# Kernel optimization log

Measured on AMD Instinct MI355X. Metric: run time of the kernel, lower is better.

The kernel has to match this reference:

```python
import jax, jax.numpy as jnp
import numpy as np

N = 50000      # nodes
E = 800000     # edges
IN = 128       # in_ch
OUT = 32       # out_ch
H = 4          # heads
ED = 16        # edge_dim
SLOPE = 0.2    # LeakyReLU negative slope (GATv2 default and outer activation)


def setup_inputs() -> dict:
    key = jax.random.key(0)
    ks = jax.random.split(key, 10)
    s_in = 1.0 / np.sqrt(IN)
    s_ed = 1.0 / np.sqrt(ED)
    s_out = 1.0 / np.sqrt(OUT)
    return {
        "x": jax.random.normal(ks[0], (N, IN), jnp.float32),
        "edge_index": jax.random.randint(ks[1], (2, E), 0, N, dtype=jnp.int32),
        "edges_attr": jax.random.normal(ks[2], (E, ED), jnp.float32),
        "W_l": jax.random.normal(ks[3], (IN, H * OUT), jnp.float32) * s_in,
        "b_l": jnp.zeros((H * OUT,), jnp.float32),
        "W_r": jax.random.normal(ks[4], (IN, H * OUT), jnp.float32) * s_in,
        "b_r": jnp.zeros((H * OUT,), jnp.float32),
        "W_e": jax.random.normal(ks[5], (ED, H * OUT), jnp.float32) * s_ed,
        "att": jax.random.normal(ks[6], (H, OUT), jnp.float32) * s_out,
        "bias": jnp.zeros((OUT,), jnp.float32),
    }


def reference(x, edge_index, edges_attr, W_l, b_l, W_r, b_r, W_e, att, bias):
    src, tgt = edge_index[0], edge_index[1]

    # add_self_loops with fill_value='mean': self-loop attr = scatter-mean of
    # incoming edge attrs per target node (0 for isolated nodes, as in PyG).
    deg = jax.ops.segment_sum(jnp.ones((E,), x.dtype), tgt, num_segments=N)
    attr_sum = jax.ops.segment_sum(edges_attr, tgt, num_segments=N)
    loop_attr = attr_sum / jnp.maximum(deg, 1.0)[:, None]
    node_ids = jnp.arange(N, dtype=src.dtype)
    src_f = jnp.concatenate([src, node_ids])   # [E+N]
    tgt_f = jnp.concatenate([tgt, node_ids])   # [E+N]
    attr_f = jnp.concatenate([edges_attr, loop_attr], axis=0)  # [E+N, ED]

    x_l = (x @ W_l + b_l).reshape(N, H, OUT)   # source transform
    x_r = (x @ W_r + b_r).reshape(N, H, OUT)   # target transform
    e = (attr_f @ W_e).reshape(-1, H, OUT)     # edge transform

    # GATv2 score: att . leaky_relu(x_l[j] + x_r[i] + e_ij)
    m = x_l[src_f] + x_r[tgt_f] + e                          # [E+N, H, OUT]
    scores = jnp.einsum('ehc,hc->eh', jax.nn.leaky_relu(m, SLOPE), att)

    # scatter-softmax over edges grouped by target node (every segment has a
    # self-loop, so segment_max is well-defined)
    smax = jax.ops.segment_max(scores, tgt_f, num_segments=N)
    ex = jnp.exp(scores - smax[tgt_f])
    denom = jax.ops.segment_sum(ex, tgt_f, num_segments=N)
    alpha = ex / denom[tgt_f]                                # [E+N, H]

    # weighted aggregation of source messages x_l[j]
    msg = alpha[:, :, None] * x_l[src_f]                     # [E+N, H, OUT]
    out = jax.ops.segment_sum(msg, tgt_f, num_segments=N)   # [N, H, OUT]

    out = out.mean(axis=1) + bias                            # concat=False -> head mean
    return jax.nn.leaky_relu(out, SLOPE)                     # outer LeakyReLU(0.2)
```

## Files before the change

### kernel.cpp

```cpp
#include <hip/hip_runtime.h>
#include <math.h>

#define NN 50000
#define NE 800000
#define SLOPE 0.2f
#define NB 49
#define GEMMB 782
#define EDGEB 3125

typedef __attribute__((ext_vector_type(8))) short bf16x8;
typedef __attribute__((ext_vector_type(4))) float f32x4;

static __device__ __forceinline__ void split_bf16(float v, unsigned short& h,
                                                  unsigned short& l) {
  unsigned u = __float_as_uint(v);
  h = (unsigned short)(u >> 16);
  float hf = __uint_as_float(((unsigned)h) << 16);
  float r = v - hf;
  l = (unsigned short)(__float_as_uint(r) >> 16);
}


__device__ __forceinline__ void gemm_body(int bx, const float* __restrict__ x,
                                          const float* __restrict__ W,
                                          const float* __restrict__ bptr,
                                          float* __restrict__ optr,
                                          unsigned short* xh_s, unsigned short* xl_s,
                                          unsigned short* wh_s, unsigned short* wl_s) {
  int tid = threadIdx.x;
  int w = tid >> 6;
  int l = tid & 63;
  int n0 = bx * 64;

  f32x4 acc[8];
#pragma unroll
  for (int i = 0; i < 8; ++i) acc[i] = (f32x4){0.f, 0.f, 0.f, 0.f};

  for (int kb = 0; kb < 128; kb += 32) {
    {
      int row = tid >> 2;
      int kc = (tid & 3) * 8;
      int gn = n0 + row;
      float4 v0 = make_float4(0.f, 0.f, 0.f, 0.f);
      float4 v1 = make_float4(0.f, 0.f, 0.f, 0.f);
      if (gn < NN) {
        v0 = *(const float4*)(x + (size_t)gn * 128 + kb + kc);
        v1 = *(const float4*)(x + (size_t)gn * 128 + kb + kc + 4);
      }
      unsigned short h[8], lo[8];
      split_bf16(v0.x, h[0], lo[0]); split_bf16(v0.y, h[1], lo[1]);
      split_bf16(v0.z, h[2], lo[2]); split_bf16(v0.w, h[3], lo[3]);
      split_bf16(v1.x, h[4], lo[4]); split_bf16(v1.y, h[5], lo[5]);
      split_bf16(v1.z, h[6], lo[6]); split_bf16(v1.w, h[7], lo[7]);
      bf16x8 hv, lv;
#pragma unroll
      for (int i = 0; i < 8; ++i) { hv[i] = (short)h[i]; lv[i] = (short)lo[i]; }
      *(bf16x8*)&xh_s[row * 40 + kc] = hv;
      *(bf16x8*)&xl_s[row * 40 + kc] = lv;
    }
    {
      int col = tid & 127;
      int kk0 = (tid >> 7) * 16;
      unsigned short h[16], lo[16];
#pragma unroll
      for (int j = 0; j < 16; ++j)
        split_bf16(W[(size_t)(kb + kk0 + j) * 128 + col], h[j], lo[j]);
      bf16x8 hv0, hv1, lv0, lv1;
#pragma unroll
      for (int i = 0; i < 8; ++i) {
        hv0[i] = (short)h[i]; hv1[i] = (short)h[8 + i];
        lv0[i] = (short)lo[i]; lv1[i] = (short)lo[8 + i];
      }
      *(bf16x8*)&wh_s[col * 40 + kk0] = hv0;
      *(bf16x8*)&wh_s[col * 40 + kk0 + 8] = hv1;
      *(bf16x8*)&wl_s[col * 40 + kk0] = lv0;
      *(bf16x8*)&wl_s[col * 40 + kk0 + 8] = lv1;
    }
    __syncthreads();

    int r16 = 16 * w + (l & 15);
    int ko = (l >> 4) * 8;
    bf16x8 ah = *(bf16x8*)&xh_s[r16 * 40 + ko];
    bf16x8 al = *(bf16x8*)&xl_s[r16 * 40 + ko];
#pragma unroll
    for (int ct = 0; ct < 8; ++ct) {
      int cbase = (ct * 16 + (l & 15)) * 40 + ko;
      bf16x8 bh = *(bf16x8*)&wh_s[cbase];
      bf16x8 bl = *(bf16x8*)&wl_s[cbase];
      acc[ct] = __builtin_amdgcn_mfma_f32_16x16x32_bf16(ah, bh, acc[ct], 0, 0, 0);
      acc[ct] = __builtin_amdgcn_mfma_f32_16x16x32_bf16(al, bh, acc[ct], 0, 0, 0);
      acc[ct] = __builtin_amdgcn_mfma_f32_16x16x32_bf16(ah, bl, acc[ct], 0, 0, 0);
    }
    __syncthreads();
  }

  int colb = l & 15;
  int rq = (l >> 4) * 4;
#pragma unroll
  for (int ct = 0; ct < 8; ++ct) {
    float bvv = bptr[ct * 16 + colb];
#pragma unroll
    for (int r = 0; r < 4; ++r) {
      int gn = n0 + 16 * w + rq + r;
      if (gn < NN) optr[(size_t)gn * 128 + ct * 16 + colb] = acc[ct][r] + bvv;
    }
  }
}


__launch_bounds__(256)
__global__ void fusedA_kernel(const float* __restrict__ x,
                              const float* __restrict__ W_l, const float* __restrict__ b_l,
                              float* __restrict__ x_l,
                              const int* __restrict__ tgt, int* __restrict__ deg,
                              int* __restrict__ rank) {
  __shared__ unsigned short xh_s[64 * 40], xl_s[64 * 40];
  __shared__ unsigned short wh_s[128 * 40], wl_s[128 * 40];
  if (blockIdx.x < GEMMB) {
    gemm_body(blockIdx.x, x, W_l, b_l, x_l, xh_s, xl_s, wh_s, wl_s);
  } else {
    int e = (blockIdx.x - GEMMB) * 256 + threadIdx.x;
    if (e < NE) rank[e] = atomicAdd(&deg[tgt[e]], 1);
  }
}


__launch_bounds__(256)
__global__ void fusedB_kernel(const float* __restrict__ x,
                              const float* __restrict__ W_r, const float* __restrict__ b_r,
                              float* __restrict__ x_r,
                              const int* __restrict__ src, const int* __restrict__ tgt,
                              const int* __restrict__ rank,
                              const int* __restrict__ rowptr,
                              const float4* __restrict__ eattr4,
                              int* __restrict__ csr_src,
                              float4* __restrict__ eattr_csr4) {
  __shared__ unsigned short xh_s[64 * 40], xl_s[64 * 40];
  __shared__ unsigned short wh_s[128 * 40], wl_s[128 * 40];
  if (blockIdx.x < GEMMB) {
    gemm_body(blockIdx.x, x, W_r, b_r, x_r, xh_s, xl_s, wh_s, wl_s);
  } else {
    int e = (blockIdx.x - GEMMB) * 256 + threadIdx.x;
    if (e < NE) {
      int t = tgt[e];
      int r = rank[e];
      float4 a0 = eattr4[(size_t)e * 4 + 0];
      float4 a1 = eattr4[(size_t)e * 4 + 1];
      float4 a2 = eattr4[(size_t)e * 4 + 2];
      float4 a3 = eattr4[(size_t)e * 4 + 3];
      int pos = rowptr[t] + r;
      csr_src[pos] = src[e];
      eattr_csr4[(size_t)pos * 4 + 0] = a0;
      eattr_csr4[(size_t)pos * 4 + 1] = a1;
      eattr_csr4[(size_t)pos * 4 + 2] = a2;
      eattr_csr4[(size_t)pos * 4 + 3] = a3;
    }
  }
}


__global__ void partial_kernel(const int* __restrict__ deg, int* __restrict__ psum) {
  int b = blockIdx.x;
  int base = b * 1024 + threadIdx.x * 4;
  int s = 0;
  if (base + 3 < NN) {
    int4 v = *(const int4*)(deg + base);
    s = v.x + v.y + v.z + v.w;
  } else {
#pragma unroll
    for (int i = 0; i < 4; ++i)
      if (base + i < NN) s += deg[base + i];
  }
  s += __shfl_xor(s, 1);
  s += __shfl_xor(s, 2);
  s += __shfl_xor(s, 4);
  s += __shfl_xor(s, 8);
  s += __shfl_xor(s, 16);
  s += __shfl_xor(s, 32);
  __shared__ int wsum[4];
  if ((threadIdx.x & 63) == 0) wsum[threadIdx.x >> 6] = s;
  __syncthreads();
  if (threadIdx.x == 0) psum[b] = wsum[0] + wsum[1] + wsum[2] + wsum[3];
}

__global__ void final_kernel(const int* __restrict__ deg, const int* __restrict__ psum,
                             int* __restrict__ rowptr) {
  __shared__ int offs_s;
  __shared__ int wtot[4];
  int b = blockIdx.x;
  int t = threadIdx.x;
  if (t < 64) {
    int lane = t;
    int mine = (lane < NB) ? psum[lane] : 0;
    int v = mine;
#pragma unroll
    for (int off = 1; off < 64; off <<= 1) {
      int u = __shfl_up(v, off);
      if (lane >= off) v += u;
    }
    if (lane == b) offs_s = v - mine;
    if (b == 0 && lane == 63) rowptr[NN] = v;
  }
  __syncthreads();

  int base = b * 1024 + t * 4;
  int d0 = 0, d1 = 0, d2 = 0, d3 = 0;
  if (base + 3 < NN) {
    int4 v = *(const int4*)(deg + base);
    d0 = v.x; d1 = v.y; d2 = v.z; d3 = v.w;
  } else {
    if (base < NN) d0 = deg[base];
    if (base + 1 < NN) d1 = deg[base + 1];
    if (base + 2 < NN) d2 = deg[base + 2];
  }
  int s = d0 + d1 + d2 + d3;
  int lane = t & 63, w = t >> 6;
  int v = s;
#pragma unroll
  for (int off = 1; off < 64; off <<= 1) {
    int u = __shfl_up(v, off);
    if (lane >= off) v += u;
  }
  if (lane == 63) wtot[w] = v;
  __syncthreads();
  int woff = 0;
#pragma unroll
  for (int i = 0; i < 4; ++i)
    if (i < w) woff += wtot[i];
  int run = offs_s + woff + (v - s);
  if (base < NN)     { rowptr[base] = run;     run += d0; }
  if (base + 1 < NN) { rowptr[base + 1] = run; run += d1; }
  if (base + 2 < NN) { rowptr[base + 2] = run; run += d2; }
  if (base + 3 < NN) { rowptr[base + 3] = run; }
}


#define EDGE_PROC(AV, XL)                                              \
  {                                                                    \
    float e0 = AV[0] * wek[0].x;                                       \
    e0 = fmaf(AV[1], wek[1].x, e0);   e0 = fmaf(AV[2], wek[2].x, e0);  \
    e0 = fmaf(AV[3], wek[3].x, e0);   e0 = fmaf(AV[4], wek[4].x, e0);  \
    e0 = fmaf(AV[5], wek[5].x, e0);   e0 = fmaf(AV[6], wek[6].x, e0);  \
    e0 = fmaf(AV[7], wek[7].x, e0);   e0 = fmaf(AV[8], wek[8].x, e0);  \
    e0 = fmaf(AV[9], wek[9].x, e0);   e0 = fmaf(AV[10], wek[10].x, e0);\
    e0 = fmaf(AV[11], wek[11].x, e0); e0 = fmaf(AV[12], wek[12].x, e0);\
    e0 = fmaf(AV[13], wek[13].x, e0); e0 = fmaf(AV[14], wek[14].x, e0);\
    e0 = fmaf(AV[15], wek[15].x, e0);                                  \
    float e1 = AV[0] * wek[0].y;                                       \
    e1 = fmaf(AV[1], wek[1].y, e1);   e1 = fmaf(AV[2], wek[2].y, e1);  \
    e1 = fmaf(AV[3], wek[3].y, e1);   e1 = fmaf(AV[4], wek[4].y, e1);  \
    e1 = fmaf(AV[5], wek[5].y, e1);   e1 = fmaf(AV[6], wek[6].y, e1);  \
    e1 = fmaf(AV[7], wek[7].y, e1);   e1 = fmaf(AV[8], wek[8].y, e1);  \
    e1 = fmaf(AV[9], wek[9].y, e1);   e1 = fmaf(AV[10], wek[10].y, e1);\
    e1 = fmaf(AV[11], wek[11].y, e1); e1 = fmaf(AV[12], wek[12].y, e1);\
    e1 = fmaf(AV[13], wek[13].y, e1); e1 = fmaf(AV[14], wek[14].y, e1);\
    e1 = fmaf(AV[15], wek[15].y, e1);                                  \
    es0 += e0; es1 += e1;                                              \
    float m0 = (XL.x + xr.x) + e0;                                     \
    float m1 = (XL.y + xr.y) + e1;                                     \
    float lm0 = fmaf(SLOPE, fminf(m0, 0.f), fmaxf(m0, 0.f));           \
    float lm1 = fmaf(SLOPE, fminf(m1, 0.f), fmaxf(m1, 0.f));           \
    float part = fmaf(attv.y, lm1, attv.x * lm0);                      \
    part += __shfl_xor(part, 1);                                       \
    part += __shfl_xor(part, 2);                                       \
    part += __shfl_xor(part, 4);                                       \
    part += __shfl_xor(part, 8);                                       \
    float p = __expf(part);                                            \
    lh += p;                                                           \
    acc0 = fmaf(p, XL.x, acc0);                                        \
    acc1 = fmaf(p, XL.y, acc1);                                        \
  }

__launch_bounds__(256)
__global__ void gat_kernel(const float* __restrict__ x_l, const float* __restrict__ x_r,
                           const int* __restrict__ rowptr, const int* __restrict__ csr_src,
                           const float* __restrict__ eattr_csr, const float* __restrict__ W_e,
                           const float* __restrict__ att, const float* __restrict__ bias,
                           float* __restrict__ out) {
  int wid = threadIdx.x >> 6;
  int lane = threadIdx.x & 63;
  int tbase = (blockIdx.x * 4 + wid) * 4;

  float2 wek[16];
#pragma unroll
  for (int k = 0; k < 16; ++k)
    wek[k] = *(const float2*)(W_e + k * 128 + 2 * lane);
  float2 attv = *(const float2*)(att + 2 * lane);
  float bv = bias[(2 * lane) & 31];
  float bv1 = bias[((2 * lane) & 31) + 1];

  for (int tt = 0; tt < 4; ++tt) {
    int t = tbase + tt;
    float2 xr = *(const float2*)(x_r + (size_t)t * 128 + 2 * lane);
    int start = __builtin_amdgcn_readfirstlane(rowptr[t]);
    int end = __builtin_amdgcn_readfirstlane(rowptr[t + 1]);

    float lh = 0.f, acc0 = 0.f, acc1 = 0.f, es0 = 0.f, es1 = 0.f;

    int j = start;
    for (; j + 4 <= end; j += 4) {
      int s0 = __builtin_amdgcn_readfirstlane(csr_src[j]);
      int s1 = __builtin_amdgcn_readfirstlane(csr_src[j + 1]);
      int s2 = __builtin_amdgcn_readfirstlane(csr_src[j + 2]);
      int s3 = __builtin_amdgcn_readfirstlane(csr_src[j + 3]);
      float2 xl0 = *(const float2*)(x_l + (size_t)s0 * 128 + 2 * lane);
      float2 xl1 = *(const float2*)(x_l + (size_t)s1 * 128 + 2 * lane);
      float2 xl2 = *(const float2*)(x_l + (size_t)s2 * 128 + 2 * lane);
      float2 xl3 = *(const float2*)(x_l + (size_t)s3 * 128 + 2 * lane);
      const float* ap0 = eattr_csr + (size_t)j * 16;
      {
        float a0[16];
#pragma unroll
        for (int k = 0; k < 16; ++k) a0[k] = ap0[k];
        EDGE_PROC(a0, xl0)
      }
      {
        float a1[16];
#pragma unroll
        for (int k = 0; k < 16; ++k) a1[k] = ap0[16 + k];
        EDGE_PROC(a1, xl1)
      }
      {
        float a2[16];
#pragma unroll
        for (int k = 0; k < 16; ++k) a2[k] = ap0[32 + k];
        EDGE_PROC(a2, xl2)
      }
      {
        float a3[16];
#pragma unroll
        for (int k = 0; k < 16; ++k) a3[k] = ap0[48 + k];
        EDGE_PROC(a3, xl3)
      }
    }
    if (j + 2 <= end) {
      int s0 = __builtin_amdgcn_readfirstlane(csr_src[j]);
      int s1 = __builtin_amdgcn_readfirstlane(csr_src[j + 1]);
      float2 xl0 = *(const float2*)(x_l + (size_t)s0 * 128 + 2 * lane);
      float2 xl1 = *(const float2*)(x_l + (size_t)s1 * 128 + 2 * lane);
      const float* ap0 = eattr_csr + (size_t)j * 16;
      {
        float a0[16];
#pragma unroll
        for (int k = 0; k < 16; ++k) a0[k] = ap0[k];
        EDGE_PROC(a0, xl0)
      }
      {
        float a1[16];
#pragma unroll
        for (int k = 0; k < 16; ++k) a1[k] = ap0[16 + k];
        EDGE_PROC(a1, xl1)
      }
      j += 2;
    }
    if (j < end) {
      int srcn = __builtin_amdgcn_readfirstlane(csr_src[j]);
      const float* ap = eattr_csr + (size_t)j * 16;
      float aC[16];
#pragma unroll
      for (int k = 0; k < 16; ++k) aC[k] = ap[k];
      float2 xlC = *(const float2*)(x_l + (size_t)srcn * 128 + 2 * lane);
      EDGE_PROC(aC, xlC)
    }

    {
      float rdeg = 1.0f / fmaxf((float)(end - start), 1.0f);
      float e0 = es0 * rdeg, e1 = es1 * rdeg;
      float2 xl = *(const float2*)(x_l + (size_t)t * 128 + 2 * lane);
      float m0 = (xl.x + xr.x) + e0;
      float m1 = (xl.y + xr.y) + e1;
      float lm0 = fmaf(SLOPE, fminf(m0, 0.f), fmaxf(m0, 0.f));
      float lm1 = fmaf(SLOPE, fminf(m1, 0.f), fmaxf(m1, 0.f));
      float part = fmaf(attv.y, lm1, attv.x * lm0);
      part += __shfl_xor(part, 1);
      part += __shfl_xor(part, 2);
      part += __shfl_xor(part, 4);
      part += __shfl_xor(part, 8);
      float p = __expf(part);
      lh += p;
      acc0 = fmaf(p, xl.x, acc0);
      acc1 = fmaf(p, xl.y, acc1);
    }

    float inv = 1.0f / lh;
    float v0 = acc0 * inv, v1 = acc1 * inv;
    v0 += __shfl_xor(v0, 16);
    v0 += __shfl_xor(v0, 32);
    v1 += __shfl_xor(v1, 16);
    v1 += __shfl_xor(v1, 32);
    if (lane < 16) {
      float o0 = fmaf(v0, 0.25f, bv);
      float o1 = fmaf(v1, 0.25f, bv1);
      o0 = fmaf(SLOPE, fminf(o0, 0.f), fmaxf(o0, 0.f));
      o1 = fmaf(SLOPE, fminf(o1, 0.f), fmaxf(o1, 0.f));
      *(float2*)(out + (size_t)t * 32 + 2 * lane) = make_float2(o0, o1);
    }
  }
}


extern "C" void kernel_launch(void* const* d_in, const int* in_sizes, int n_in,
                              void* d_out, int out_size, void* d_ws, size_t ws_size,
                              hipStream_t stream) {
  const float* x = (const float*)d_in[0];
  const int* ei = (const int*)d_in[1];
  const float* eattr = (const float*)d_in[2];
  const float* W_l = (const float*)d_in[3];
  const float* b_l = (const float*)d_in[4];
  const float* W_r = (const float*)d_in[5];
  const float* b_r = (const float*)d_in[6];
  const float* W_e = (const float*)d_in[7];
  const float* att = (const float*)d_in[8];
  const float* bias = (const float*)d_in[9];
  float* out = (float*)d_out;

  char* ws = (char*)d_ws;
  int* csr_src = (int*)ws;
  float* eattr_csr = (float*)(ws + 3200000);
  float* x_l = (float*)(ws + 54400000);
  float* x_r = (float*)(ws + 80000000);
  int* deg = (int*)(ws + 105600000);
  int* rowptr = (int*)(ws + 105800000);
  int* rank = (int*)(ws + 106000016);
  int* psum = (int*)(ws + 109200016);

  hipMemsetAsync(deg, 0, NN * sizeof(int), stream);
  fusedA_kernel<<<GEMMB + EDGEB, 256, 0, stream>>>(x, W_l, b_l, x_l, ei + NE, deg, rank);
  partial_kernel<<<NB, 256, 0, stream>>>(deg, psum);
  final_kernel<<<NB, 256, 0, stream>>>(deg, psum, rowptr);
  fusedB_kernel<<<GEMMB + EDGEB, 256, 0, stream>>>(
      x, W_r, b_r, x_r, ei, ei + NE, rank, rowptr, (const float4*)eattr,
      csr_src, (float4*)eattr_csr);
  gat_kernel<<<NN / 16, 256, 0, stream>>>(x_l, x_r, rowptr, csr_src, eattr_csr, W_e, att, bias, out);
}
```

Before: 308.5 us.

## Build CSR of (src, edge id) pairs instead of permuting edge attributes

The CSR build no longer copies 64-byte edge attribute rows into target-sorted order. Instead it stores (source, original edge id) pairs, with slots claimed by an atomic cursor, and the attention kernel gathers attributes from the original array by edge id. This removes the rank array and a full permuted write of the attributes, in exchange for random reads of attributes in the gat kernel and a non-deterministic edge order within each segment. Separately, the GEMM now loads A fragments straight from global memory into registers, dropping the x tiles from shared memory.

```diff
diff --git a/kernel.cpp b/kernel.cpp
--- a/kernel.cpp
+++ b/kernel.cpp
@@ -25,39 +25,22 @@
                                           const float* __restrict__ W,
                                           const float* __restrict__ bptr,
                                           float* __restrict__ optr,
-                                          unsigned short* xh_s, unsigned short* xl_s,
                                           unsigned short* wh_s, unsigned short* wl_s) {
   int tid = threadIdx.x;
   int w = tid >> 6;
   int l = tid & 63;
   int n0 = bx * 64;
 
+  int arow = n0 + 16 * w + (l & 15);
+  if (arow >= NN) arow = NN - 1;
+  int ko = (l >> 4) * 8;
+  const float* xp = x + (size_t)arow * 128 + ko;
+
   f32x4 acc[8];
 #pragma unroll
   for (int i = 0; i < 8; ++i) acc[i] = (f32x4){0.f, 0.f, 0.f, 0.f};
 
   for (int kb = 0; kb < 128; kb += 32) {
-    {
-      int row = tid >> 2;
-      int kc = (tid & 3) * 8;
-      int gn = n0 + row;
-      float4 v0 = make_float4(0.f, 0.f, 0.f, 0.f);
-      float4 v1 = make_float4(0.f, 0.f, 0.f, 0.f);
-      if (gn < NN) {
-        v0 = *(const float4*)(x + (size_t)gn * 128 + kb + kc);
-        v1 = *(const float4*)(x + (size_t)gn * 128 + kb + kc + 4);
-      }
-      unsigned short h[8], lo[8];
-      split_bf16(v0.x, h[0], lo[0]); split_bf16(v0.y, h[1], lo[1]);
-      split_bf16(v0.z, h[2], lo[2]); split_bf16(v0.w, h[3], lo[3]);
-      split_bf16(v1.x, h[4], lo[4]); split_bf16(v1.y, h[5], lo[5]);
-      split_bf16(v1.z, h[6], lo[6]); split_bf16(v1.w, h[7], lo[7]);
-      bf16x8 hv, lv;
-#pragma unroll
-      for (int i = 0; i < 8; ++i) { hv[i] = (short)h[i]; lv[i] = (short)lo[i]; }
-      *(bf16x8*)&xh_s[row * 40 + kc] = hv;
-      *(bf16x8*)&xl_s[row * 40 + kc] = lv;
-    }
     {
       int col = tid & 127;
       int kk0 = (tid >> 7) * 16;
@@ -76,12 +59,18 @@
       *(bf16x8*)&wl_s[col * 40 + kk0] = lv0;
       *(bf16x8*)&wl_s[col * 40 + kk0 + 8] = lv1;
     }
+    float4 v0 = *(const float4*)(xp + kb);
+    float4 v1 = *(const float4*)(xp + kb + 4);
+    unsigned short h[8], lo[8];
+    split_bf16(v0.x, h[0], lo[0]); split_bf16(v0.y, h[1], lo[1]);
+    split_bf16(v0.z, h[2], lo[2]); split_bf16(v0.w, h[3], lo[3]);
+    split_bf16(v1.x, h[4], lo[4]); split_bf16(v1.y, h[5], lo[5]);
+    split_bf16(v1.z, h[6], lo[6]); split_bf16(v1.w, h[7], lo[7]);
+    bf16x8 ah, al;
+#pragma unroll
+    for (int i = 0; i < 8; ++i) { ah[i] = (short)h[i]; al[i] = (short)lo[i]; }
     __syncthreads();
 
-    int r16 = 16 * w + (l & 15);
-    int ko = (l >> 4) * 8;
-    bf16x8 ah = *(bf16x8*)&xh_s[r16 * 40 + ko];
-    bf16x8 al = *(bf16x8*)&xl_s[r16 * 40 + ko];
 #pragma unroll
     for (int ct = 0; ct < 8; ++ct) {
       int cbase = (ct * 16 + (l & 15)) * 40 + ko;
@@ -112,15 +101,13 @@
 __global__ void fusedA_kernel(const float* __restrict__ x,
                               const float* __restrict__ W_l, const float* __restrict__ b_l,
                               float* __restrict__ x_l,
-                              const int* __restrict__ tgt, int* __restrict__ deg,
-                              int* __restrict__ rank) {
-  __shared__ unsigned short xh_s[64 * 40], xl_s[64 * 40];
+                              const int* __restrict__ tgt, int* __restrict__ deg) {
   __shared__ unsigned short wh_s[128 * 40], wl_s[128 * 40];
   if (blockIdx.x < GEMMB) {
-    gemm_body(blockIdx.x, x, W_l, b_l, x_l, xh_s, xl_s, wh_s, wl_s);
+    gemm_body(blockIdx.x, x, W_l, b_l, x_l, wh_s, wl_s);
   } else {
     int e = (blockIdx.x - GEMMB) * 256 + threadIdx.x;
-    if (e < NE) rank[e] = atomicAdd(&deg[tgt[e]], 1);
+    if (e < NE) atomicAdd(&deg[tgt[e]], 1);
   }
 }
 
@@ -130,30 +117,16 @@
                               const float* __restrict__ W_r, const float* __restrict__ b_r,
                               float* __restrict__ x_r,
                               const int* __restrict__ src, const int* __restrict__ tgt,
-                              const int* __restrict__ rank,
-                              const int* __restrict__ rowptr,
-                              const float4* __restrict__ eattr4,
-                              int* __restrict__ csr_src,
-                              float4* __restrict__ eattr_csr4) {
-  __shared__ unsigned short xh_s[64 * 40], xl_s[64 * 40];
+                              int* __restrict__ cursor, int2* __restrict__ csr) {
   __shared__ unsigned short wh_s[128 * 40], wl_s[128 * 40];
   if (blockIdx.x < GEMMB) {
-    gemm_body(blockIdx.x, x, W_r, b_r, x_r, xh_s, xl_s, wh_s, wl_s);
+    gemm_body(blockIdx.x, x, W_r, b_r, x_r, wh_s, wl_s);
   } else {
     int e = (blockIdx.x - GEMMB) * 256 + threadIdx.x;
     if (e < NE) {
       int t = tgt[e];
-      int r = rank[e];
-      float4 a0 = eattr4[(size_t)e * 4 + 0];
-      float4 a1 = eattr4[(size_t)e * 4 + 1];
-      float4 a2 = eattr4[(size_t)e * 4 + 2];
-      float4 a3 = eattr4[(size_t)e * 4 + 3];
-      int pos = rowptr[t] + r;
-      csr_src[pos] = src[e];
-      eattr_csr4[(size_t)pos * 4 + 0] = a0;
-      eattr_csr4[(size_t)pos * 4 + 1] = a1;
-      eattr_csr4[(size_t)pos * 4 + 2] = a2;
-      eattr_csr4[(size_t)pos * 4 + 3] = a3;
+      int pos = atomicAdd(&cursor[t], 1);
+      csr[pos] = make_int2(src[e], e);
     }
   }
 }
@@ -184,7 +157,7 @@
 }
 
 __global__ void final_kernel(const int* __restrict__ deg, const int* __restrict__ psum,
-                             int* __restrict__ rowptr) {
+                             int* __restrict__ rowptr, int* __restrict__ cursor) {
   __shared__ int offs_s;
   __shared__ int wtot[4];
   int b = blockIdx.x;
@@ -228,10 +201,10 @@
   for (int i = 0; i < 4; ++i)
     if (i < w) woff += wtot[i];
   int run = offs_s + woff + (v - s);
-  if (base < NN)     { rowptr[base] = run;     run += d0; }
-  if (base + 1 < NN) { rowptr[base + 1] = run; run += d1; }
-  if (base + 2 < NN) { rowptr[base + 2] = run; run += d2; }
-  if (base + 3 < NN) { rowptr[base + 3] = run; }
+  if (base < NN)     { rowptr[base] = run;     cursor[base] = run;     run += d0; }
+  if (base + 1 < NN) { rowptr[base + 1] = run; cursor[base + 1] = run; run += d1; }
+  if (base + 2 < NN) { rowptr[base + 2] = run; cursor[base + 2] = run; run += d2; }
+  if (base + 3 < NN) { rowptr[base + 3] = run; cursor[base + 3] = run; }
 }
 
 
@@ -273,8 +246,8 @@
 
 __launch_bounds__(256)
 __global__ void gat_kernel(const float* __restrict__ x_l, const float* __restrict__ x_r,
-                           const int* __restrict__ rowptr, const int* __restrict__ csr_src,
-                           const float* __restrict__ eattr_csr, const float* __restrict__ W_e,
+                           const int* __restrict__ rowptr, const int2* __restrict__ csr,
+                           const float* __restrict__ eattr, const float* __restrict__ W_e,
                            const float* __restrict__ att, const float* __restrict__ bias,
                            float* __restrict__ out) {
   int wid = threadIdx.x >> 6;
@@ -299,63 +272,65 @@
 
     int j = start;
     for (; j + 4 <= end; j += 4) {
-      int s0 = __builtin_amdgcn_readfirstlane(csr_src[j]);
-      int s1 = __builtin_amdgcn_readfirstlane(csr_src[j + 1]);
-      int s2 = __builtin_amdgcn_readfirstlane(csr_src[j + 2]);
-      int s3 = __builtin_amdgcn_readfirstlane(csr_src[j + 3]);
+      int2 ce0 = csr[j];
+      int2 ce1 = csr[j + 1];
+      int2 ce2 = csr[j + 2];
+      int2 ce3 = csr[j + 3];
+      int s0 = __builtin_amdgcn_readfirstlane(ce0.x);
+      int d0i = __builtin_amdgcn_readfirstlane(ce0.y);
+      int s1 = __builtin_amdgcn_readfirstlane(ce1.x);
+      int d1i = __builtin_amdgcn_readfirstlane(ce1.y);
+      int s2 = __builtin_amdgcn_readfirstlane(ce2.x);
+      int d2i = __builtin_amdgcn_readfirstlane(ce2.y);
+      int s3 = __builtin_amdgcn_readfirstlane(ce3.x);
+      int d3i = __builtin_amdgcn_readfirstlane(ce3.y);
       float2 xl0 = *(const float2*)(x_l + (size_t)s0 * 128 + 2 * lane);
       float2 xl1 = *(const float2*)(x_l + (size_t)s1 * 128 + 2 * lane);
       float2 xl2 = *(const float2*)(x_l + (size_t)s2 * 128 + 2 * lane);
       float2 xl3 = *(const float2*)(x_l + (size_t)s3 * 128 + 2 * lane);
-      const float* ap0 = eattr_csr + (size_t)j * 16;
-      {
-        float a0[16];
-#pragma unroll
-        for (int k = 0; k < 16; ++k) a0[k] = ap0[k];
-        EDGE_PROC(a0, xl0)
-      }
-      {
-        float a1[16];
-#pragma unroll
-        for (int k = 0; k < 16; ++k) a1[k] = ap0[16 + k];
-        EDGE_PROC(a1, xl1)
-      }
-      {
-        float a2[16];
-#pragma unroll
-        for (int k = 0; k < 16; ++k) a2[k] = ap0[32 + k];
-        EDGE_PROC(a2, xl2)
-      }
-      {
-        float a3[16];
-#pragma unroll
-        for (int k = 0; k < 16; ++k) a3[k] = ap0[48 + k];
-        EDGE_PROC(a3, xl3)
-      }
+      const float* ap0 = eattr + (size_t)d0i * 16;
+      const float* ap1 = eattr + (size_t)d1i * 16;
+      const float* ap2 = eattr + (size_t)d2i * 16;
+      const float* ap3 = eattr + (size_t)d3i * 16;
+      float a0[16], a1[16], a2[16], a3[16];
+#pragma unroll
+      for (int k = 0; k < 16; ++k) a0[k] = ap0[k];
+#pragma unroll
+      for (int k = 0; k < 16; ++k) a1[k] = ap1[k];
+#pragma unroll
+      for (int k = 0; k < 16; ++k) a2[k] = ap2[k];
+#pragma unroll
+      for (int k = 0; k < 16; ++k) a3[k] = ap3[k];
+      EDGE_PROC(a0, xl0)
+      EDGE_PROC(a1, xl1)
+      EDGE_PROC(a2, xl2)
+      EDGE_PROC(a3, xl3)
     }
     if (j + 2 <= end) {
-      int s0 = __builtin_amdgcn_readfirstlane(csr_src[j]);
-      int s1 = __builtin_amdgcn_readfirstlane(csr_src[j + 1]);
-      float2 xl0 = *(const float2*)(x_l + (size_t)s0 * 128 + 2 * lane);
-      float2 xl1 = *(const float2*)(x_l + (size_t)s1 * 128 + 2 * lane);
-      const float* ap0 = eattr_csr + (size_t)j * 16;
-      {
-        float a0[16];
-#pragma unroll
-        for (int k = 0; k < 16; ++k) a0[k] = ap0[k];
-        EDGE_PROC(a0, xl0)
-      }
-      {
-        float a1[16];
-#pragma unroll
-        for (int k = 0; k < 16; ++k) a1[k] = ap0[16 + k];
-        EDGE_PROC(a1, xl1)
-      }
+      int2 ceA = csr[j];
+      int2 ceB = csr[j + 1];
+      int srcA = __builtin_amdgcn_readfirstlane(ceA.x);
+      int eidA = __builtin_amdgcn_readfirstlane(ceA.y);
+      int srcB = __builtin_amdgcn_readfirstlane(ceB.x);
+      int eidB = __builtin_amdgcn_readfirstlane(ceB.y);
+      const float* apA = eattr + (size_t)eidA * 16;
+      const float* apB = eattr + (size_t)eidB * 16;
+      float aA[16], aB[16];
+#pragma unroll
+      for (int k = 0; k < 16; ++k) aA[k] = apA[k];
+#pragma unroll
+      for (int k = 0; k < 16; ++k) aB[k] = apB[k];
+      float2 xlA = *(const float2*)(x_l + (size_t)srcA * 128 + 2 * lane);
+      float2 xlB = *(const float2*)(x_l + (size_t)srcB * 128 + 2 * lane);
+      EDGE_PROC(aA, xlA)
+      EDGE_PROC(aB, xlB)
       j += 2;
     }
     if (j < end) {
-      int srcn = __builtin_amdgcn_readfirstlane(csr_src[j]);
-      const float* ap = eattr_csr + (size_t)j * 16;
+      int2 ce = csr[j];
+      int srcn = __builtin_amdgcn_readfirstlane(ce.x);
+      int eid = __builtin_amdgcn_readfirstlane(ce.y);
+      const float* ap = eattr + (size_t)eid * 16;
       float aC[16];
 #pragma unroll
       for (int k = 0; k < 16; ++k) aC[k] = ap[k];
@@ -415,21 +390,18 @@
   float* out = (float*)d_out;
 
   char* ws = (char*)d_ws;
-  int* csr_src = (int*)ws;
-  float* eattr_csr = (float*)(ws + 3200000);
-  float* x_l = (float*)(ws + 54400000);
-  float* x_r = (float*)(ws + 80000000);
-  int* deg = (int*)(ws + 105600000);
-  int* rowptr = (int*)(ws + 105800000);
-  int* rank = (int*)(ws + 106000016);
-  int* psum = (int*)(ws + 109200016);
+  int2* csr = (int2*)ws;
+  float* x_l = (float*)(ws + 6400000);
+  float* x_r = (float*)(ws + 32000000);
+  int* deg = (int*)(ws + 57600000);
+  int* rowptr = (int*)(ws + 57800000);
+  int* cursor = (int*)(ws + 58000016);
+  int* psum = (int*)(ws + 58200016);
 
   hipMemsetAsync(deg, 0, NN * sizeof(int), stream);
-  fusedA_kernel<<<GEMMB + EDGEB, 256, 0, stream>>>(x, W_l, b_l, x_l, ei + NE, deg, rank);
+  fusedA_kernel<<<GEMMB + EDGEB, 256, 0, stream>>>(x, W_l, b_l, x_l, ei + NE, deg);
   partial_kernel<<<NB, 256, 0, stream>>>(deg, psum);
-  final_kernel<<<NB, 256, 0, stream>>>(deg, psum, rowptr);
-  fusedB_kernel<<<GEMMB + EDGEB, 256, 0, stream>>>(
-      x, W_r, b_r, x_r, ei, ei + NE, rank, rowptr, (const float4*)eattr,
-      csr_src, (float4*)eattr_csr);
-  gat_kernel<<<NN / 16, 256, 0, stream>>>(x_l, x_r, rowptr, csr_src, eattr_csr, W_e, att, bias, out);
-}
+  final_kernel<<<NB, 256, 0, stream>>>(deg, psum, rowptr, cursor);
+  fusedB_kernel<<<GEMMB + EDGEB, 256, 0, stream>>>(x, W_r, b_r, x_r, ei, ei + NE, cursor, csr);
+  gat_kernel<<<NN / 16, 256, 0, stream>>>(x_l, x_r, rowptr, csr, eattr, W_e, att, bias, out);
+}
```

New measurement: 342.7 us. 11.1% more time.
